# Performance work log

Measured on AMD Instinct MI355X. Metric: run time of the kernel, lower is better.

The kernel has to match this reference:

```python
import jax, jax.numpy as jnp
import numpy as np

D_MODEL, N_LEVELS, N_HEADS, N_POINTS = 256, 4, 8, 4
HEAD_DIM = D_MODEL // N_HEADS
SPATIAL = [(100, 100), (50, 50), (25, 25), (13, 13)]  # (H, W) per level
BATCH = 2


def setup_inputs() -> dict:
    key = jax.random.key(0)
    ks = jax.random.split(key, 10)
    len_in = sum(h * w for h, w in SPATIAL)
    n, lq = BATCH, len_in
    s = 0.02
    mlp = N_HEADS * N_LEVELS * N_POINTS
    starts = np.cumsum([0] + [h * w for h, w in SPATIAL])[:-1]
    return {
        "query": jax.random.normal(ks[0], (n, lq, D_MODEL), jnp.float32),
        "reference_points": jax.random.uniform(ks[1], (n, lq, N_LEVELS, 2), jnp.float32),
        "input_flatten": jax.random.normal(ks[2], (n, len_in, D_MODEL), jnp.float32),
        "input_spatial_shapes": jnp.array(SPATIAL, dtype=jnp.int32),
        "input_level_start_index": jnp.array(starts, dtype=jnp.int32),
        "Wv": jax.random.normal(ks[3], (D_MODEL, D_MODEL), jnp.float32) * s,
        "bv": jnp.zeros((D_MODEL,), jnp.float32),
        "Woff": jax.random.normal(ks[4], (D_MODEL, mlp * 2), jnp.float32) * s,
        "boff": jax.random.normal(ks[5], (mlp * 2,), jnp.float32) * s,
        "Wattn": jax.random.normal(ks[6], (D_MODEL, mlp), jnp.float32) * s,
        "battn": jnp.zeros((mlp,), jnp.float32),
        "Wout": jax.random.normal(ks[7], (D_MODEL, D_MODEL), jnp.float32) * s,
        "bout": jnp.zeros((D_MODEL,), jnp.float32),
    }


def _ms_deform_attn_core(value, spatial_shapes, loc, aw):
    """value [N,S,M,D]; loc [N,Lq,M,L,P,2] in [0,1]; aw [N,Lq,M,L,P] -> [N,Lq,M*D].
    Faithful to F.grid_sample(mode='bilinear', padding_mode='zeros', align_corners=False)."""
    n, lq, m, L, p, _ = loc.shape
    d = value.shape[-1]
    out = jnp.zeros((n, m, lq, d), value.dtype)
    gather = jax.vmap(jax.vmap(lambda v, i: v[i]))  # vmap over N and M
    start = 0
    for lvl, (H, W) in enumerate(spatial_shapes):
        v = value[:, start:start + H * W].transpose(0, 2, 1, 3)  # [N,M,HW,D]
        start += H * W
        # align_corners=False: grid g=2*loc-1 -> pixel = ((g+1)*size-1)/2 = loc*size-0.5
        x = loc[:, :, :, lvl, :, 0] * W - 0.5  # [N,Lq,M,P]
        y = loc[:, :, :, lvl, :, 1] * H - 0.5
        x0 = jnp.floor(x)
        y0 = jnp.floor(y)
        wx = x - x0
        wy = y - y0
        x0i = x0.astype(jnp.int32)
        y0i = y0.astype(jnp.int32)
        samp = jnp.zeros((n, m, lq * p, d), value.dtype)
        for dy, wyc in ((0, 1.0 - wy), (1, wy)):
            for dx, wxc in ((0, 1.0 - wx), (1, wx)):
                xi = x0i + dx
                yi = y0i + dy
                valid = (xi >= 0) & (xi < W) & (yi >= 0) & (yi < H)  # zeros padding
                idx = jnp.clip(yi, 0, H - 1) * W + jnp.clip(xi, 0, W - 1)
                idx = idx.transpose(0, 2, 1, 3).reshape(n, m, lq * p)
                w = (wxc * wyc * valid).transpose(0, 2, 1, 3).reshape(n, m, lq * p)
                samp = samp + gather(v, idx) * w[..., None]
        samp = samp.reshape(n, m, lq, p, d)
        aw_l = aw[:, :, :, lvl, :].transpose(0, 2, 1, 3)  # [N,M,Lq,P]
        out = out + (samp * aw_l[..., None]).sum(3)
    return out.transpose(0, 2, 1, 3).reshape(n, lq, m * d)


def reference(query, reference_points, input_flatten, input_spatial_shapes,
              input_level_start_index, Wv, bv, Woff, boff, Wattn, battn, Wout, bout):
    n, lq, _ = query.shape
    m, L, p = N_HEADS, N_LEVELS, N_POINTS
    shapes = np.asarray(input_spatial_shapes)  # concrete/static [L,2] = (H,W)
    value = (input_flatten @ Wv + bv).reshape(n, -1, m, HEAD_DIM)
    off = (query @ Woff + boff).reshape(n, lq, m, L, p, 2)
    aw = jax.nn.softmax((query @ Wattn + battn).reshape(n, lq, m, L * p), axis=-1)
    aw = aw.reshape(n, lq, m, L, p)
    norm = jnp.asarray(shapes[:, ::-1].astype(np.float32))  # [L,2] = (W,H)
    loc = reference_points[:, :, None, :, None, :] + off / norm[None, None, None, :, None, :]
    out = _ms_deform_attn_core(value, [tuple(s) for s in shapes.tolist()], loc, aw)
    return out @ Wout + bout
```

## Files before the change

kernel.cpp:

```cpp
#include <hip/hip_runtime.h>
#include <hip/hip_bf16.h>

#define NB    2
#define LQ    13294
#define DM    256
#define NH    8
#define HD    32
#define NL    4
#define NP    4
#define ROWS  (NB*LQ)

#define OFF_VALUE 0u
#define OFF_TMP   13613056u
#define OFF_OFFS  27226112u
#define OFF_AWL   54452224u
#define OFF_WT    61258752u
#define OFF_FLAG  61717504u

#define WT_WV    0
#define WT_WOFF  65536
#define WT_WATTN 131072
#define WT_WOUT  163840

typedef __attribute__((ext_vector_type(8))) short short8;
typedef __attribute__((ext_vector_type(4))) float floatx4;

static __device__ __forceinline__ float blo(int u)  { return __uint_as_float(((unsigned)u) << 16); }
static __device__ __forceinline__ float bhif(int u) { return __uint_as_float(((unsigned)u) & 0xffff0000u); }

static __device__ __forceinline__ int pack_bf2(float a, float b) {
    __hip_bfloat162 h(__float2bfloat16(a), __float2bfloat16(b));
    int u; __builtin_memcpy(&u, &h, 4); return u;
}

static __device__ __forceinline__ void gload_lds16(const void* g, void* l) {
    __builtin_amdgcn_global_load_lds(
        (const __attribute__((address_space(1))) unsigned*)g,
        (__attribute__((address_space(3))) unsigned*)l, 16, 0, 0);
}

__global__ void sniff_k(const unsigned int* __restrict__ q, int* __restrict__ flag) {
    const int t = threadIdx.x;
    int hits = 0;
#pragma unroll
    for (int i = 0; i < 4; ++i) {
        unsigned lo = q[t * 4 + i] & 0xffffu;
        unsigned e  = (lo >> 7) & 0xffu;
        if ((e >= 110u && e <= 132u) || lo == 0u) ++hits;
    }
#pragma unroll
    for (int s = 1; s < 64; s <<= 1) hits += __shfl_xor(hits, s);
    if (t == 0) *flag = (hits > 160) ? 1 : 0;
}

__global__ __launch_bounds__(256) void trans_k(
    const void* __restrict__ s0, const void* __restrict__ s1,
    const void* __restrict__ s2, const void* __restrict__ s3,
    short* __restrict__ wt, const int* __restrict__ flagp)
{
    const int flag = *flagp;
    const int z = blockIdx.z;
    const void* src = (z == 0) ? s0 : (z == 1) ? s1 : (z == 2) ? s2 : s3;
    short* dst = wt + ((z == 0) ? WT_WV : (z == 1) ? WT_WOFF : (z == 2) ? WT_WATTN : WT_WOUT);
    const int N = (z == 2) ? 128 : 256;
    const int n0 = blockIdx.x * 32, k0 = blockIdx.y * 32;
    if (n0 >= N) return;

    __shared__ short tile[32 * 36];
    const int t = threadIdx.x;
    const int r = t >> 3, c4 = (t & 7) * 4;
    if (flag) {
        const short* sp = (const short*)src + (k0 + r) * N + n0 + c4;
        *(short4*)&tile[r * 36 + c4] = *(const short4*)sp;
    } else {
        const float* sp = (const float*)src + (k0 + r) * N + n0 + c4;
        float4 v = *(const float4*)sp;
        short4 o;
        o.x = (short)(pack_bf2(v.x, v.x) & 0xffff);
        o.y = (short)(pack_bf2(v.y, v.y) & 0xffff);
        o.z = (short)(pack_bf2(v.z, v.z) & 0xffff);
        o.w = (short)(pack_bf2(v.w, v.w) & 0xffff);
        *(short4*)&tile[r * 36 + c4] = o;
    }
    __syncthreads();
    const int nn = t >> 3, r4 = (t & 7) * 4;
    short4 o;
    o.x = tile[(r4 + 0) * 36 + nn];
    o.y = tile[(r4 + 1) * 36 + nn];
    o.z = tile[(r4 + 2) * 36 + nn];
    o.w = tile[(r4 + 3) * 36 + nn];
    *(short4*)&dst[(n0 + nn) * 256 + k0 + r4] = o;
}

static __device__ __forceinline__ void gemm_body(
    const void* __restrict__ A, const short* __restrict__ Wt,
    const void* __restrict__ bias, const void* __restrict__ bias2,
    void* __restrict__ C, void* __restrict__ C2,
    const int M, const int Nn, const bool a_bf, const int c_mode,
    const int flag, const int bx, const int by,
    short* __restrict__ As, short* __restrict__ Bs)
{
    const int tid = threadIdx.x;
    const int w = tid >> 6, lane = tid & 63;
    const int qd = lane >> 4, ln = lane & 15;
    const int bm = by * 128, bn = bx * 128;
    const int wm = (w & 1) * 64, wn = (w >> 1) * 64;

    const int ar0 = tid >> 2,         ak0 = (tid & 3) * 8;
    const int ar1 = (tid + 256) >> 2, ak1 = (tid & 3) * 8;
    const int ga0 = min(bm + ar0, M - 1), ga1 = min(bm + ar1, M - 1);
    short* lA0 = As + w * 512;
    short* lA1 = As + 2048 + w * 512;
    short* lB0 = Bs + w * 512;
    short* lB1 = Bs + 2048 + w * 512;

    floatx4 acc[4][4];
#pragma unroll
    for (int i = 0; i < 4; ++i)
#pragma unroll
        for (int j = 0; j < 4; ++j) acc[i][j] = floatx4{0.f, 0.f, 0.f, 0.f};

    const short* Ab = (const short*)A;
    const float* Af = (const float*)A;

    for (int k0 = 0; k0 < 256; k0 += 32) {
        __syncthreads();
        gload_lds16(Wt + (bn + ar0) * 256 + k0 + ak0, lB0);
        gload_lds16(Wt + (bn + ar1) * 256 + k0 + ak1, lB1);
        if (a_bf) {
            gload_lds16(Ab + ga0 * 256 + k0 + ak0, lA0);
            gload_lds16(Ab + ga1 * 256 + k0 + ak1, lA1);
        } else {
            float4 f0 = *(const float4*)(Af + ga0 * 256 + k0 + ak0);
            float4 f1 = *(const float4*)(Af + ga0 * 256 + k0 + ak0 + 4);
            int4 p0; p0.x = pack_bf2(f0.x, f0.y); p0.y = pack_bf2(f0.z, f0.w);
                     p0.z = pack_bf2(f1.x, f1.y); p0.w = pack_bf2(f1.z, f1.w);
            *(int4*)&As[ar0 * 32 + ak0] = p0;
            float4 g0 = *(const float4*)(Af + ga1 * 256 + k0 + ak1);
            float4 g1 = *(const float4*)(Af + ga1 * 256 + k0 + ak1 + 4);
            int4 p1; p1.x = pack_bf2(g0.x, g0.y); p1.y = pack_bf2(g0.z, g0.w);
                     p1.z = pack_bf2(g1.x, g1.y); p1.w = pack_bf2(g1.z, g1.w);
            *(int4*)&As[ar1 * 32 + ak1] = p1;
        }
        __syncthreads();

        short8 af[4], bf[4];
#pragma unroll
        for (int i = 0; i < 4; ++i)
            af[i] = *(const short8*)&As[(wm + i * 16 + ln) * 32 + qd * 8];
#pragma unroll
        for (int j = 0; j < 4; ++j)
            bf[j] = *(const short8*)&Bs[(wn + j * 16 + ln) * 32 + qd * 8];
#pragma unroll
        for (int i = 0; i < 4; ++i)
#pragma unroll
            for (int j = 0; j < 4; ++j)
                acc[i][j] = __builtin_amdgcn_mfma_f32_16x16x32_bf16(af[i], bf[j], acc[i][j], 0, 0, 0);
    }

#pragma unroll
    for (int j = 0; j < 4; ++j) {
        const int col = bn + wn + j * 16 + ln;
        float bj;
        if (c_mode == 3 && col >= 256) {
            if (flag) bj = __bfloat162float(((const __hip_bfloat16*)bias2)[col - 256]);
            else      bj = ((const float*)bias2)[col - 256];
        } else {
            if (flag) bj = __bfloat162float(((const __hip_bfloat16*)bias)[col]);
            else      bj = ((const float*)bias)[col];
        }
#pragma unroll
        for (int i = 0; i < 4; ++i) {
#pragma unroll
            for (int r = 0; r < 4; ++r) {
                const int row = bm + wm + i * 16 + qd * 4 + r;
                if (row >= M) continue;
                const float v = acc[i][j][r] + bj;
                if (c_mode == 0)      ((__hip_bfloat16*)C)[row * Nn + col] = __float2bfloat16(v);
                else if (c_mode == 1) ((float*)C)[row * Nn + col] = v;
                else if (c_mode == 2) {
                    if (flag) ((__hip_bfloat16*)C)[row * Nn + col] = __float2bfloat16(v);
                    else      ((float*)C)[row * Nn + col] = v;
                } else {
                    if (col < 256) ((float*)C)[row * 256 + col] = v;
                    else           ((__hip_bfloat16*)C2)[row * 128 + col - 256] = __float2bfloat16(v);
                }
            }
        }
    }
}

__global__ __launch_bounds__(256) void gemm_lds_k(
    const void* __restrict__ A, const short* __restrict__ Wt,
    const void* __restrict__ bias, const void* __restrict__ bias2,
    void* __restrict__ C, void* __restrict__ C2,
    int M, int Nn, int a_mode, int c_mode, const int* __restrict__ flagp)
{
    __shared__ __align__(16) short As[128 * 32];
    __shared__ __align__(16) short Bs[128 * 32];
    const int flag = *flagp;
    const bool a_bf = (a_mode == 2) ? (flag != 0) : true;
    gemm_body(A, Wt, bias, bias2, C, C2, M, Nn, a_bf, c_mode, flag,
              blockIdx.x, blockIdx.y, As, Bs);
}

__global__ __launch_bounds__(256) void gemm_fused_k(
    const void* __restrict__ flat, const void* __restrict__ query,
    const short* __restrict__ wt,
    const void* __restrict__ bv, const void* __restrict__ boff,
    const void* __restrict__ battn,
    void* __restrict__ value, void* __restrict__ offsb, void* __restrict__ awl,
    const int* __restrict__ flagp)
{
    __shared__ __align__(16) short As[128 * 32];
    __shared__ __align__(16) short Bs[128 * 32];
    const int flag = *flagp;
    const bool a_bf = (flag != 0);
    if (blockIdx.z == 0) {
        if (blockIdx.x >= 2) return;
        gemm_body(flat, wt + WT_WV, bv, nullptr, value, nullptr,
                  ROWS, 256, a_bf, 0, flag, blockIdx.x, blockIdx.y, As, Bs);
    } else {
        gemm_body(query, wt + WT_WOFF, boff, battn, offsb, awl,
                  ROWS, 384, a_bf, 3, flag, blockIdx.x, blockIdx.y, As, Bs);
    }
}

__global__ __launch_bounds__(256) void sampler_k(
    const void* __restrict__ refp, const short* __restrict__ value,
    const float* __restrict__ offs, const short* __restrict__ awl,
    short* __restrict__ tmp, const int* __restrict__ flagp)
{
    const int flag = *flagp;
    const int wq = threadIdx.x >> 6;
    const int nq = blockIdx.x * 4 + wq;
    const int lane = threadIdx.x & 63;
    const int h = lane >> 3, u = lane & 7;
    const int n = (nq >= LQ) ? 1 : 0;

    __shared__ int2 recs[4][16][9][5];

    const int lg = *(const int*)(awl + nq * 128 + h * 16 + u * 2);
    float l0 = blo(lg), l1 = bhif(lg);
    float m = fmaxf(l0, l1);
    m = fmaxf(m, __shfl_xor(m, 1));
    m = fmaxf(m, __shfl_xor(m, 2));
    m = fmaxf(m, __shfl_xor(m, 4));
    float e0 = __expf(l0 - m), e1 = __expf(l1 - m);
    float s = e0 + e1;
    s += __shfl_xor(s, 1);
    s += __shfl_xor(s, 2);
    s += __shfl_xor(s, 4);
    const float inv = 1.f / s;
    const float w0 = e0 * inv, w1 = e1 * inv;

    const float4 of = *(const float4*)(offs + nq * 256 + h * 32 + u * 4);

    float rxl, ryl;
    if (flag) {
        const int rr = *(const int*)((const short*)refp + nq * 8 + (u & 3) * 2);
        rxl = blo(rr); ryl = bhif(rr);
    } else {
        const float* rp = (const float*)refp + nq * 8 + (u & 3) * 2;
        rxl = rp[0]; ryl = rp[1];
    }

    const int l = u >> 1;
    const int Wl = (0x0D193264 >> (l * 8)) & 0xff;
    const int St = (l == 0) ? 0 : (l == 1) ? 10000 : (l == 2) ? 12500 : 13125;
    const int rowbase = n * LQ + St;
    const float Wf = (float)Wl;
    const float rx = __shfl(rxl, h * 8 + l);
    const float ry = __shfl(ryl, h * 8 + l);

#pragma unroll
    for (int j = 0; j < 2; ++j) {
        const float ox = j ? of.z : of.x;
        const float oy = j ? of.w : of.y;
        const float wa = j ? w1 : w0;
        const float px = fmaf(rx, Wf, ox) - 0.5f;
        const float py = fmaf(ry, Wf, oy) - 0.5f;
        const float x0f = floorf(px), y0f = floorf(py);
        const float wx = px - x0f, wy = py - y0f;
        const int x0 = (int)x0f, y0 = (int)y0f;
        const float wxc[2] = {1.f - wx, wx};
        const float wyc[2] = {1.f - wy, wy};
#pragma unroll
        for (int dy = 0; dy < 2; ++dy) {
#pragma unroll
            for (int dx = 0; dx < 2; ++dx) {
                const int xi = x0 + dx, yi = y0 + dy;
                const bool vld = ((unsigned)xi < (unsigned)Wl) & ((unsigned)yi < (unsigned)Wl);
                int row = rowbase + yi * Wl + xi;
                row = vld ? row : rowbase;
                const float ww = vld ? wa * wxc[dx] * wyc[dy] : 0.f;
                recs[wq][u * 2 + j][h][dy * 2 + dx] =
                    make_int2(row << 9, __float_as_int(ww));
            }
        }
    }

    __syncthreads();

    const int laneoff = h * 64 + u * 8;
    const char* vb = (const char*)value;
    float a0 = 0.f, a1 = 0.f, a2 = 0.f, a3 = 0.f;

    int2  rA[8], rB[8];
    float wA[8], wB[8];

#define CHUNK(RW, WW, kk)                                                 \
    _Pragma("unroll")                                                     \
    for (int j = 0; j < 8; ++j) {                                         \
        const int2 rr = recs[wq][(kk) * 2 + (j >> 2)][h][j & 3];          \
        WW[j] = __int_as_float(rr.y);                                     \
        RW[j] = *(const int2*)(vb + (unsigned)(rr.x + laneoff));          \
    }
#define EAT(RW, WW)                                                       \
    _Pragma("unroll")                                                     \
    for (int j = 0; j < 8; ++j) {                                         \
        a0 = fmaf(WW[j], blo(RW[j].x),  a0);                              \
        a1 = fmaf(WW[j], bhif(RW[j].x), a1);                              \
        a2 = fmaf(WW[j], blo(RW[j].y),  a2);                              \
        a3 = fmaf(WW[j], bhif(RW[j].y), a3);                              \
    }

    CHUNK(rA, wA, 0)
    CHUNK(rB, wB, 1)
    EAT(rA, wA)  CHUNK(rA, wA, 2)
    EAT(rB, wB)  CHUNK(rB, wB, 3)
    EAT(rA, wA)  CHUNK(rA, wA, 4)
    EAT(rB, wB)  CHUNK(rB, wB, 5)
    EAT(rA, wA)  CHUNK(rA, wA, 6)
    EAT(rB, wB)  CHUNK(rB, wB, 7)
    EAT(rA, wA)
    EAT(rB, wB)
#undef CHUNK
#undef EAT

    int2 o;
    o.x = pack_bf2(a0, a1);
    o.y = pack_bf2(a2, a3);
    *(int2*)(tmp + nq * 256 + h * 32 + u * 4) = o;
}

extern "C" void kernel_launch(void* const* d_in, const int* in_sizes, int n_in,
                              void* d_out, int out_size, void* d_ws, size_t ws_size,
                              hipStream_t stream)
{
    const void* query  = d_in[0];
    const void* refpts = d_in[1];
    const void* flat   = d_in[2];
    const void* Wv     = d_in[5];
    const void* bv     = d_in[6];
    const void* Woff   = d_in[7];
    const void* boff   = d_in[8];
    const void* Wattn  = d_in[9];
    const void* battn  = d_in[10];
    const void* Wout   = d_in[11];
    const void* bout   = d_in[12];

    char* ws = (char*)d_ws;
    short* value = (short*)(ws + OFF_VALUE);
    short* tmp   = (short*)(ws + OFF_TMP);
    float* offsb = (float*)(ws + OFF_OFFS);
    short* awl   = (short*)(ws + OFF_AWL);
    short* wt    = (short*)(ws + OFF_WT);
    int*   flagp = (int*)(ws + OFF_FLAG);

    const int gmy = (ROWS + 127) / 128;

    sniff_k<<<1, 64, 0, stream>>>((const unsigned int*)query, flagp);
    trans_k<<<dim3(8, 8, 4), 256, 0, stream>>>(Wv, Woff, Wattn, Wout, wt, flagp);
    gemm_fused_k<<<dim3(3, gmy, 2), 256, 0, stream>>>(flat, query, wt, bv, boff, battn,
                                                      value, offsb, awl, flagp);
    sampler_k<<<ROWS / 4, 256, 0, stream>>>(refpts, value, offsb, awl, tmp, flagp);
    gemm_lds_k<<<dim3(2, gmy), 256, 0, stream>>>(tmp, wt + WT_WOUT, bout, nullptr,
                                                 d_out, nullptr, ROWS, 256, 1, 2, flagp);
}
```

Baseline: 229.3 us.

## Fuse all stages into one persistent cooperative kernel with grid syncs

Replaces the five separate launches (sniff, weight transpose, fused input GEMMs, sampler, output GEMM) with one cooperative persistent kernel that loops over work items and separates the stages with grid-wide syncs. Stage bodies are factored into device functions that share one LDS buffer. The aim is to remove per-launch overhead and inter-kernel gaps. In exchange, occupancy is capped at the occupancy-derived block count, grid syncs add their own cost, and the grid-stride loops may balance work worse than the original launches did; the multi-kernel path stays as a fallback.

New measurement: 231.5 us. Within noise of the previous version (+0.9%).

```diff
diff --git a/kernel.cpp b/kernel.cpp
--- a/kernel.cpp
+++ b/kernel.cpp
@@ -1,5 +1,8 @@
 #include <hip/hip_runtime.h>
 #include <hip/hip_bf16.h>
+#include <hip/hip_cooperative_groups.h>
+
+namespace cg = cooperative_groups;
 
 #define NB    2
 #define LQ    13294
@@ -39,8 +42,8 @@
         (__attribute__((address_space(3))) unsigned*)l, 16, 0, 0);
 }
 
-__global__ void sniff_k(const unsigned int* __restrict__ q, int* __restrict__ flag) {
-    const int t = threadIdx.x;
+static __device__ __forceinline__ void sniff_core(const unsigned* __restrict__ q,
+                                                  int* __restrict__ flag, int t) {
     int hits = 0;
 #pragma unroll
     for (int i = 0; i < 4; ++i) {
@@ -53,20 +56,21 @@
     if (t == 0) *flag = (hits > 160) ? 1 : 0;
 }
 
-__global__ __launch_bounds__(256) void trans_k(
+__global__ void sniff_k(const unsigned int* __restrict__ q, int* __restrict__ flag) {
+    sniff_core(q, flag, threadIdx.x);
+}
+
+static __device__ __forceinline__ void trans_core(
+    int z, int bx, int by, int flag,
     const void* __restrict__ s0, const void* __restrict__ s1,
     const void* __restrict__ s2, const void* __restrict__ s3,
-    short* __restrict__ wt, const int* __restrict__ flagp)
-{
-    const int flag = *flagp;
-    const int z = blockIdx.z;
+    short* __restrict__ wt, short* __restrict__ tile )
+{
     const void* src = (z == 0) ? s0 : (z == 1) ? s1 : (z == 2) ? s2 : s3;
     short* dst = wt + ((z == 0) ? WT_WV : (z == 1) ? WT_WOFF : (z == 2) ? WT_WATTN : WT_WOUT);
     const int N = (z == 2) ? 128 : 256;
-    const int n0 = blockIdx.x * 32, k0 = blockIdx.y * 32;
-    if (n0 >= N) return;
-
-    __shared__ short tile[32 * 36];
+    const int n0 = bx * 32, k0 = by * 32;
+
     const int t = threadIdx.x;
     const int r = t >> 3, c4 = (t & 7) * 4;
     if (flag) {
@@ -90,6 +94,18 @@
     o.z = tile[(r4 + 2) * 36 + nn];
     o.w = tile[(r4 + 3) * 36 + nn];
     *(short4*)&dst[(n0 + nn) * 256 + k0 + r4] = o;
+}
+
+__global__ __launch_bounds__(256) void trans_k(
+    const void* __restrict__ s0, const void* __restrict__ s1,
+    const void* __restrict__ s2, const void* __restrict__ s3,
+    short* __restrict__ wt, const int* __restrict__ flagp)
+{
+    __shared__ short tile[32 * 36];
+    const int z = blockIdx.z;
+    const int N = (z == 2) ? 128 : 256;
+    if ((int)blockIdx.x * 32 >= N) return;
+    trans_core(z, blockIdx.x, blockIdx.y, *flagp, s0, s1, s2, s3, wt, tile);
 }
 
 static __device__ __forceinline__ void gemm_body(
@@ -226,19 +242,14 @@
     }
 }
 
-__global__ __launch_bounds__(256) void sampler_k(
+static __device__ __forceinline__ void sampler_core(
+    const int nq, const int lane, const int flag,
     const void* __restrict__ refp, const short* __restrict__ value,
     const float* __restrict__ offs, const short* __restrict__ awl,
-    short* __restrict__ tmp, const int* __restrict__ flagp)
-{
-    const int flag = *flagp;
-    const int wq = threadIdx.x >> 6;
-    const int nq = blockIdx.x * 4 + wq;
-    const int lane = threadIdx.x & 63;
+    short* __restrict__ tmp, int2* __restrict__ recs)
+{
     const int h = lane >> 3, u = lane & 7;
     const int n = (nq >= LQ) ? 1 : 0;
-
-    __shared__ int2 recs[4][16][9][5];
 
     const int lg = *(const int*)(awl + nq * 128 + h * 16 + u * 2);
     float l0 = blo(lg), l1 = bhif(lg);
@@ -294,7 +305,7 @@
                 int row = rowbase + yi * Wl + xi;
                 row = vld ? row : rowbase;
                 const float ww = vld ? wa * wxc[dx] * wyc[dy] : 0.f;
-                recs[wq][u * 2 + j][h][dy * 2 + dx] =
+                recs[((u * 2 + j) * 9 + h) * 5 + dy * 2 + dx] =
                     make_int2(row << 9, __float_as_int(ww));
             }
         }
@@ -312,7 +323,7 @@
 #define CHUNK(RW, WW, kk)                                                 \
     _Pragma("unroll")                                                     \
     for (int j = 0; j < 8; ++j) {                                         \
-        const int2 rr = recs[wq][(kk) * 2 + (j >> 2)][h][j & 3];          \
+        const int2 rr = recs[(((kk) * 2 + (j >> 2)) * 9 + h) * 5 + (j & 3)]; \
         WW[j] = __int_as_float(rr.y);                                     \
         RW[j] = *(const int2*)(vb + (unsigned)(rr.x + laneoff));          \
     }
@@ -344,6 +355,81 @@
     *(int2*)(tmp + nq * 256 + h * 32 + u * 4) = o;
 }
 
+__global__ __launch_bounds__(256) void sampler_k(
+    const void* __restrict__ refp, const short* __restrict__ value,
+    const float* __restrict__ offs, const short* __restrict__ awl,
+    short* __restrict__ tmp, const int* __restrict__ flagp)
+{
+    __shared__ int2 recs[4][16][9][5];
+    const int wq = threadIdx.x >> 6;
+    sampler_core(blockIdx.x * 4 + wq, threadIdx.x & 63, *flagp,
+                 refp, value, offs, awl, tmp, &recs[wq][0][0][0]);
+}
+
+__global__ __launch_bounds__(256) void mega_k(
+    const void* __restrict__ query, const void* __restrict__ refpts,
+    const void* __restrict__ flat,
+    const void* __restrict__ Wv,   const void* __restrict__ bv,
+    const void* __restrict__ Woff, const void* __restrict__ boff,
+    const void* __restrict__ Wattn,const void* __restrict__ battn,
+    const void* __restrict__ Wout, const void* __restrict__ bout,
+    void* __restrict__ dout, char* __restrict__ ws)
+{
+    __shared__ __align__(16) char smem[23040];
+
+    short* value = (short*)(ws + OFF_VALUE);
+    short* tmp   = (short*)(ws + OFF_TMP);
+    float* offsb = (float*)(ws + OFF_OFFS);
+    short* awl   = (short*)(ws + OFF_AWL);
+    short* wt    = (short*)(ws + OFF_WT);
+    int*   flagp = (int*)(ws + OFF_FLAG);
+
+    const int bid = blockIdx.x, G = gridDim.x, tid = threadIdx.x;
+    cg::grid_group gg = cg::this_grid();
+
+    if (bid == 0 && tid < 64) sniff_core((const unsigned*)query, flagp, tid);
+    gg.sync();
+    const int flag = *flagp;
+
+    for (int j = bid; j < 224; j += G) {
+        int z, x, y;
+        if (j < 64)       { z = 0; x = j & 7;         y = j >> 3; }
+        else if (j < 128) { z = 1; x = (j - 64) & 7;  y = (j - 64) >> 3; }
+        else if (j < 160) { z = 2; x = (j - 128) & 3; y = (j - 128) >> 2; }
+        else              { z = 3; x = (j - 160) & 7; y = (j - 160) >> 3; }
+        trans_core(z, x, y, flag, Wv, Woff, Wattn, Wout, wt, (short*)smem);
+        __syncthreads();
+    }
+    gg.sync();
+
+    short* As = (short*)smem;
+    short* Bs = (short*)(smem + 8192);
+    const bool a_bf = (flag != 0);
+    for (int j = bid; j < 1040; j += G) {
+        if (j < 416) {
+            gemm_body(flat, wt + WT_WV, bv, nullptr, value, nullptr,
+                      ROWS, 256, a_bf, 0, flag, j & 1, j >> 1, As, Bs);
+        } else {
+            const int t2 = j - 416;
+            gemm_body(query, wt + WT_WOFF, boff, battn, offsb, awl,
+                      ROWS, 384, a_bf, 3, flag, t2 % 3, t2 / 3, As, Bs);
+        }
+    }
+    gg.sync();
+
+    {
+        int2* recbase = (int2*)smem + (tid >> 6) * (16 * 9 * 5);
+        const int wq = tid >> 6, lane = tid & 63;
+        for (int j = bid; j < ROWS / 4; j += G)
+            sampler_core(j * 4 + wq, lane, flag, refpts, value, offsb, awl, tmp, recbase);
+    }
+    gg.sync();
+
+    for (int j = bid; j < 416; j += G)
+        gemm_body(tmp, wt + WT_WOUT, bout, nullptr, dout, nullptr,
+                  ROWS, 256, true, 2, flag, j & 1, j >> 1, As, Bs);
+}
+
 extern "C" void kernel_launch(void* const* d_in, const int* in_sizes, int n_in,
                               void* d_out, int out_size, void* d_ws, size_t ws_size,
                               hipStream_t stream)
@@ -368,8 +454,32 @@
     short* wt    = (short*)(ws + OFF_WT);
     int*   flagp = (int*)(ws + OFF_FLAG);
 
+    static int gblocks = 0;
+    if (gblocks == 0) {
+        int nb = 0;
+        hipError_t qe = hipOccupancyMaxActiveBlocksPerMultiprocessor(
+            &nb, reinterpret_cast<const void*>(&mega_k), 256, 0);
+        if (qe != hipSuccess || nb < 1) gblocks = -1;
+        else {
+            gblocks = nb * 256;
+            if (gblocks > 2048) gblocks = 2048;
+        }
+    }
+
+    if (gblocks > 0) {
+        void* args[] = {
+            (void*)&query, (void*)&refpts, (void*)&flat,
+            (void*)&Wv, (void*)&bv, (void*)&Woff, (void*)&boff,
+            (void*)&Wattn, (void*)&battn, (void*)&Wout, (void*)&bout,
+            (void*)&d_out, (void*)&ws };
+        hipError_t e = hipLaunchCooperativeKernel(
+            reinterpret_cast<const void*>(&mega_k),
+            dim3((unsigned)gblocks), dim3(256), args, 0, stream);
+        if (e == hipSuccess) return;
+        gblocks = -1;
+    }
+
     const int gmy = (ROWS + 127) / 128;
-
     sniff_k<<<1, 64, 0, stream>>>((const unsigned int*)query, flagp);
     trans_k<<<dim3(8, 8, 4), 256, 0, stream>>>(Wv, Woff, Wattn, Wout, wt, flagp);
     gemm_fused_k<<<dim3(3, gmy, 2), 256, 0, stream>>>(flat, query, wt, bv, boff, battn,
```

## Double-buffer GEMM LDS staging and pre-convert fp32 inputs to bf16

Applied to the files above, without the earlier changes.

The GEMM main loop now uses two LDS buffers and issues the loads for the next K-slice before computing on the current one, which cuts one barrier per iteration and overlaps memory with MFMA. When the workspace is large enough, a new conv_k kernel first converts the fp32 flat and query inputs to bf16. The input GEMMs can then use direct global-to-LDS loads instead of converting in registers. This adds an extra pass over both inputs and doubles LDS use per block, which may lower occupancy.

New measurement: 235.9 us. 1.03x slower.

```diff
diff --git a/kernel.cpp b/kernel.cpp
--- a/kernel.cpp
+++ b/kernel.cpp
@@ -16,6 +16,9 @@
 #define OFF_AWL   54452224u
 #define OFF_WT    61258752u
 #define OFF_FLAG  61717504u
+#define OFF_FBF   61717632u
+#define OFF_QBF   75330688u
+#define WS_NEED   88943744u
 
 #define WT_WV    0
 #define WT_WOFF  65536
@@ -51,6 +54,25 @@
 #pragma unroll
     for (int s = 1; s < 64; s <<= 1) hits += __shfl_xor(hits, s);
     if (t == 0) *flag = (hits > 160) ? 1 : 0;
+}
+
+__global__ __launch_bounds__(256) void conv_k(
+    const float* __restrict__ fa, const float* __restrict__ fb,
+    short* __restrict__ oa, short* __restrict__ ob,
+    const int* __restrict__ flagp)
+{
+    if (*flagp) return;
+    const int total = ROWS * 256 / 8;
+    for (int i = blockIdx.x * 256 + threadIdx.x; i < total; i += gridDim.x * 256) {
+        float4 a0 = ((const float4*)fa)[i * 2], a1 = ((const float4*)fa)[i * 2 + 1];
+        int4 p; p.x = pack_bf2(a0.x, a0.y); p.y = pack_bf2(a0.z, a0.w);
+                p.z = pack_bf2(a1.x, a1.y); p.w = pack_bf2(a1.z, a1.w);
+        ((int4*)oa)[i] = p;
+        float4 b0 = ((const float4*)fb)[i * 2], b1 = ((const float4*)fb)[i * 2 + 1];
+        int4 q; q.x = pack_bf2(b0.x, b0.y); q.y = pack_bf2(b0.z, b0.w);
+                q.z = pack_bf2(b1.x, b1.y); q.w = pack_bf2(b1.z, b1.w);
+        ((int4*)ob)[i] = q;
+    }
 }
 
 __global__ __launch_bounds__(256) void trans_k(
@@ -96,9 +118,10 @@
     const void* __restrict__ A, const short* __restrict__ Wt,
     const void* __restrict__ bias, const void* __restrict__ bias2,
     void* __restrict__ C, void* __restrict__ C2,
-    const int M, const int Nn, const bool a_bf, const int c_mode,
+    const int M, const int Nn, const bool stage_f32, const int c_mode,
     const int flag, const int bx, const int by,
-    short* __restrict__ As, short* __restrict__ Bs)
+    short* __restrict__ As0, short* __restrict__ As1,
+    short* __restrict__ Bs0, short* __restrict__ Bs1)
 {
     const int tid = threadIdx.x;
     const int w = tid >> 6, lane = tid & 63;
@@ -106,13 +129,9 @@
     const int bm = by * 128, bn = bx * 128;
     const int wm = (w & 1) * 64, wn = (w >> 1) * 64;
 
-    const int ar0 = tid >> 2,         ak0 = (tid & 3) * 8;
-    const int ar1 = (tid + 256) >> 2, ak1 = (tid & 3) * 8;
+    const int ar0 = tid >> 2, ar1 = ar0 + 64;
+    const int ak  = (tid & 3) * 8;
     const int ga0 = min(bm + ar0, M - 1), ga1 = min(bm + ar1, M - 1);
-    short* lA0 = As + w * 512;
-    short* lA1 = As + 2048 + w * 512;
-    short* lB0 = Bs + w * 512;
-    short* lB1 = Bs + 2048 + w * 512;
 
     floatx4 acc[4][4];
 #pragma unroll
@@ -123,39 +142,50 @@
     const short* Ab = (const short*)A;
     const float* Af = (const float*)A;
 
-    for (int k0 = 0; k0 < 256; k0 += 32) {
-        __syncthreads();
-        gload_lds16(Wt + (bn + ar0) * 256 + k0 + ak0, lB0);
-        gload_lds16(Wt + (bn + ar1) * 256 + k0 + ak1, lB1);
-        if (a_bf) {
-            gload_lds16(Ab + ga0 * 256 + k0 + ak0, lA0);
-            gload_lds16(Ab + ga1 * 256 + k0 + ak1, lA1);
+    auto stage = [&](int kk, short* Ad, short* Bd) {
+        const int k0 = kk * 32;
+        gload_lds16(Wt + (bn + ar0) * 256 + k0 + ak, Bd + w * 512);
+        gload_lds16(Wt + (bn + ar1) * 256 + k0 + ak, Bd + 2048 + w * 512);
+        if (!stage_f32) {
+            gload_lds16(Ab + ga0 * 256 + k0 + ak, Ad + w * 512);
+            gload_lds16(Ab + ga1 * 256 + k0 + ak, Ad + 2048 + w * 512);
         } else {
-            float4 f0 = *(const float4*)(Af + ga0 * 256 + k0 + ak0);
-            float4 f1 = *(const float4*)(Af + ga0 * 256 + k0 + ak0 + 4);
+            float4 f0 = *(const float4*)(Af + ga0 * 256 + k0 + ak);
+            float4 f1 = *(const float4*)(Af + ga0 * 256 + k0 + ak + 4);
             int4 p0; p0.x = pack_bf2(f0.x, f0.y); p0.y = pack_bf2(f0.z, f0.w);
                      p0.z = pack_bf2(f1.x, f1.y); p0.w = pack_bf2(f1.z, f1.w);
-            *(int4*)&As[ar0 * 32 + ak0] = p0;
-            float4 g0 = *(const float4*)(Af + ga1 * 256 + k0 + ak1);
-            float4 g1 = *(const float4*)(Af + ga1 * 256 + k0 + ak1 + 4);
+            *(int4*)&Ad[ar0 * 32 + ak] = p0;
+            float4 g0 = *(const float4*)(Af + ga1 * 256 + k0 + ak);
+            float4 g1 = *(const float4*)(Af + ga1 * 256 + k0 + ak + 4);
             int4 p1; p1.x = pack_bf2(g0.x, g0.y); p1.y = pack_bf2(g0.z, g0.w);
                      p1.z = pack_bf2(g1.x, g1.y); p1.w = pack_bf2(g1.z, g1.w);
-            *(int4*)&As[ar1 * 32 + ak1] = p1;
+            *(int4*)&Ad[ar1 * 32 + ak] = p1;
         }
-        __syncthreads();
-
-        short8 af[4], bf[4];
+    };
+
+    stage(0, As0, Bs0);
+    __syncthreads();
+
+#pragma unroll
+    for (int kk = 0; kk < 8; ++kk) {
+        short* Ac = (kk & 1) ? As1 : As0;
+        short* Bc = (kk & 1) ? Bs1 : Bs0;
+        if (kk < 7) stage(kk + 1, (kk & 1) ? As0 : As1, (kk & 1) ? Bs0 : Bs1);
+
+        short8 af[4], bfr[4];
 #pragma unroll
         for (int i = 0; i < 4; ++i)
-            af[i] = *(const short8*)&As[(wm + i * 16 + ln) * 32 + qd * 8];
+            af[i] = *(const short8*)&Ac[(wm + i * 16 + ln) * 32 + qd * 8];
 #pragma unroll
         for (int j = 0; j < 4; ++j)
-            bf[j] = *(const short8*)&Bs[(wn + j * 16 + ln) * 32 + qd * 8];
+            bfr[j] = *(const short8*)&Bc[(wn + j * 16 + ln) * 32 + qd * 8];
 #pragma unroll
         for (int i = 0; i < 4; ++i)
 #pragma unroll
             for (int j = 0; j < 4; ++j)
-                acc[i][j] = __builtin_amdgcn_mfma_f32_16x16x32_bf16(af[i], bf[j], acc[i][j], 0, 0, 0);
+                acc[i][j] = __builtin_amdgcn_mfma_f32_16x16x32_bf16(af[i], bfr[j], acc[i][j], 0, 0, 0);
+
+        if (kk < 7) __syncthreads();
     }
 
 #pragma unroll
@@ -194,35 +224,36 @@
     const void* __restrict__ A, const short* __restrict__ Wt,
     const void* __restrict__ bias, const void* __restrict__ bias2,
     void* __restrict__ C, void* __restrict__ C2,
-    int M, int Nn, int a_mode, int c_mode, const int* __restrict__ flagp)
-{
-    __shared__ __align__(16) short As[128 * 32];
-    __shared__ __align__(16) short Bs[128 * 32];
-    const int flag = *flagp;
-    const bool a_bf = (a_mode == 2) ? (flag != 0) : true;
-    gemm_body(A, Wt, bias, bias2, C, C2, M, Nn, a_bf, c_mode, flag,
-              blockIdx.x, blockIdx.y, As, Bs);
+    int M, int Nn, int c_mode, const int* __restrict__ flagp)
+{
+    __shared__ __align__(16) short As0[4096], As1[4096], Bs0[4096], Bs1[4096];
+    gemm_body(A, Wt, bias, bias2, C, C2, M, Nn, false, c_mode, *flagp,
+              blockIdx.x, blockIdx.y, As0, As1, Bs0, Bs1);
 }
 
 __global__ __launch_bounds__(256) void gemm_fused_k(
-    const void* __restrict__ flat, const void* __restrict__ query,
+    const void* __restrict__ flat, const void* __restrict__ flatbf,
+    const void* __restrict__ query, const void* __restrict__ querybf,
     const short* __restrict__ wt,
     const void* __restrict__ bv, const void* __restrict__ boff,
     const void* __restrict__ battn,
     void* __restrict__ value, void* __restrict__ offsb, void* __restrict__ awl,
-    const int* __restrict__ flagp)
-{
-    __shared__ __align__(16) short As[128 * 32];
-    __shared__ __align__(16) short Bs[128 * 32];
+    int big, const int* __restrict__ flagp)
+{
+    __shared__ __align__(16) short As0[4096], As1[4096], Bs0[4096], Bs1[4096];
     const int flag = *flagp;
-    const bool a_bf = (flag != 0);
+    const bool stage_f32 = (!flag) && (!big);
     if (blockIdx.z == 0) {
         if (blockIdx.x >= 2) return;
-        gemm_body(flat, wt + WT_WV, bv, nullptr, value, nullptr,
-                  ROWS, 256, a_bf, 0, flag, blockIdx.x, blockIdx.y, As, Bs);
+        const void* A = flag ? flat : (big ? flatbf : flat);
+        gemm_body(A, wt + WT_WV, bv, nullptr, value, nullptr,
+                  ROWS, 256, stage_f32, 0, flag, blockIdx.x, blockIdx.y,
+                  As0, As1, Bs0, Bs1);
     } else {
-        gemm_body(query, wt + WT_WOFF, boff, battn, offsb, awl,
-                  ROWS, 384, a_bf, 3, flag, blockIdx.x, blockIdx.y, As, Bs);
+        const void* A = flag ? query : (big ? querybf : query);
+        gemm_body(A, wt + WT_WOFF, boff, battn, offsb, awl,
+                  ROWS, 384, stage_f32, 3, flag, blockIdx.x, blockIdx.y,
+                  As0, As1, Bs0, Bs1);
     }
 }
 
@@ -293,9 +324,8 @@
                 const bool vld = ((unsigned)xi < (unsigned)Wl) & ((unsigned)yi < (unsigned)Wl);
                 int row = rowbase + yi * Wl + xi;
                 row = vld ? row : rowbase;
-                const float ww = vld ? wa * wxc[dx] * wyc[dy] : 0.f;
                 recs[wq][u * 2 + j][h][dy * 2 + dx] =
-                    make_int2(row << 9, __float_as_int(ww));
+                    make_int2(row << 9, __float_as_int(vld ? wa * wxc[dx] * wyc[dy] : 0.f));
             }
         }
     }
@@ -367,14 +397,21 @@
     short* awl   = (short*)(ws + OFF_AWL);
     short* wt    = (short*)(ws + OFF_WT);
     int*   flagp = (int*)(ws + OFF_FLAG);
-
+    short* fbf   = (short*)(ws + OFF_FBF);
+    short* qbf   = (short*)(ws + OFF_QBF);
+
+    const int big = (ws_size >= (size_t)WS_NEED) ? 1 : 0;
     const int gmy = (ROWS + 127) / 128;
 
     sniff_k<<<1, 64, 0, stream>>>((const unsigned int*)query, flagp);
+    if (big)
+        conv_k<<<1664, 256, 0, stream>>>((const float*)flat, (const float*)query,
+                                         fbf, qbf, flagp);
     trans_k<<<dim3(8, 8, 4), 256, 0, stream>>>(Wv, Woff, Wattn, Wout, wt, flagp);
-    gemm_fused_k<<<dim3(3, gmy, 2), 256, 0, stream>>>(flat, query, wt, bv, boff, battn,
-                                                      value, offsb, awl, flagp);
+    gemm_fused_k<<<dim3(3, gmy, 2), 256, 0, stream>>>(flat, fbf, query, qbf, wt,
+                                                      bv, boff, battn,
+                                                      value, offsb, awl, big, flagp);
     sampler_k<<<ROWS / 4, 256, 0, stream>>>(refpts, value, offsb, awl, tmp, flagp);
     gemm_lds_k<<<dim3(2, gmy), 256, 0, stream>>>(tmp, wt + WT_WOUT, bout, nullptr,
-                                                 d_out, nullptr, ROWS, 256, 1, 2, flagp);
-}
+                                                 d_out, nullptr, ROWS, 256, 2, flagp);
+}
```

## Replace LDS-tiled 128x128 GEMMs with single-wave 32x64 register-direct MFMA GEMM

Applied to the files above, without the earlier changes.

Replaces the shared-memory tiled 256-thread GEMM (128x128 tiles, global_load_lds staging, barriers) with a 64-thread kernel that loads A and B fragments directly from global memory into registers and computes 32x64 tiles. The fused value/offset projection launch is split into two separate launches, and the output projection uses the same kernel. The intent is to remove LDS staging and barrier overhead and to raise the block count for better occupancy. In exchange, global-memory traffic rises because there is no LDS reuse and the weight matrix is re-read per small tile.

Result: slower. 283.2 us (+23.5%).

```diff
diff --git a/kernel.cpp b/kernel.cpp
--- a/kernel.cpp
+++ b/kernel.cpp
@@ -31,12 +31,6 @@
 static __device__ __forceinline__ int pack_bf2(float a, float b) {
     __hip_bfloat162 h(__float2bfloat16(a), __float2bfloat16(b));
     int u; __builtin_memcpy(&u, &h, 4); return u;
-}
-
-static __device__ __forceinline__ void gload_lds16(const void* g, void* l) {
-    __builtin_amdgcn_global_load_lds(
-        (const __attribute__((address_space(1))) unsigned*)g,
-        (__attribute__((address_space(3))) unsigned*)l, 16, 0, 0);
 }
 
 __global__ void sniff_k(const unsigned int* __restrict__ q, int* __restrict__ flag) {
@@ -92,75 +86,73 @@
     *(short4*)&dst[(n0 + nn) * 256 + k0 + r4] = o;
 }
 
-static __device__ __forceinline__ void gemm_body(
+static __device__ __forceinline__ short8 ldA_f32(const float* p) {
+    float4 f0 = *(const float4*)p, f1 = *(const float4*)(p + 4);
+    int4 q; q.x = pack_bf2(f0.x, f0.y); q.y = pack_bf2(f0.z, f0.w);
+            q.z = pack_bf2(f1.x, f1.y); q.w = pack_bf2(f1.z, f1.w);
+    short8 r; __builtin_memcpy(&r, &q, 16); return r;
+}
+
+__global__ __launch_bounds__(64) void wgemm_k(
     const void* __restrict__ A, const short* __restrict__ Wt,
     const void* __restrict__ bias, const void* __restrict__ bias2,
     void* __restrict__ C, void* __restrict__ C2,
-    const int M, const int Nn, const bool a_bf, const int c_mode,
-    const int flag, const int bx, const int by,
-    short* __restrict__ As, short* __restrict__ Bs)
+    int M, int Nn, int a_mode, int c_mode, const int* __restrict__ flagp)
 {
-    const int tid = threadIdx.x;
-    const int w = tid >> 6, lane = tid & 63;
+    const int flag = *flagp;
+    const bool a_bf = (a_mode == 1) || (flag != 0);
+    const int lane = threadIdx.x;
     const int qd = lane >> 4, ln = lane & 15;
-    const int bm = by * 128, bn = bx * 128;
-    const int wm = (w & 1) * 64, wn = (w >> 1) * 64;
-
-    const int ar0 = tid >> 2,         ak0 = (tid & 3) * 8;
-    const int ar1 = (tid + 256) >> 2, ak1 = (tid & 3) * 8;
-    const int ga0 = min(bm + ar0, M - 1), ga1 = min(bm + ar1, M - 1);
-    short* lA0 = As + w * 512;
-    short* lA1 = As + 2048 + w * 512;
-    short* lB0 = Bs + w * 512;
-    short* lB1 = Bs + 2048 + w * 512;
-
-    floatx4 acc[4][4];
-#pragma unroll
-    for (int i = 0; i < 4; ++i)
-#pragma unroll
-        for (int j = 0; j < 4; ++j) acc[i][j] = floatx4{0.f, 0.f, 0.f, 0.f};
-
+    const int bm = blockIdx.y * 32, bn = blockIdx.x * 64;
+
+    const int ar0 = min(bm + ln, M - 1);
+    const int ar1 = min(bm + 16 + ln, M - 1);
     const short* Ab = (const short*)A;
     const float* Af = (const float*)A;
 
-    for (int k0 = 0; k0 < 256; k0 += 32) {
-        __syncthreads();
-        gload_lds16(Wt + (bn + ar0) * 256 + k0 + ak0, lB0);
-        gload_lds16(Wt + (bn + ar1) * 256 + k0 + ak1, lB1);
-        if (a_bf) {
-            gload_lds16(Ab + ga0 * 256 + k0 + ak0, lA0);
-            gload_lds16(Ab + ga1 * 256 + k0 + ak1, lA1);
-        } else {
-            float4 f0 = *(const float4*)(Af + ga0 * 256 + k0 + ak0);
-            float4 f1 = *(const float4*)(Af + ga0 * 256 + k0 + ak0 + 4);
-            int4 p0; p0.x = pack_bf2(f0.x, f0.y); p0.y = pack_bf2(f0.z, f0.w);
-                     p0.z = pack_bf2(f1.x, f1.y); p0.w = pack_bf2(f1.z, f1.w);
-            *(int4*)&As[ar0 * 32 + ak0] = p0;
-            float4 g0 = *(const float4*)(Af + ga1 * 256 + k0 + ak1);
-            float4 g1 = *(const float4*)(Af + ga1 * 256 + k0 + ak1 + 4);
-            int4 p1; p1.x = pack_bf2(g0.x, g0.y); p1.y = pack_bf2(g0.z, g0.w);
-                     p1.z = pack_bf2(g1.x, g1.y); p1.w = pack_bf2(g1.z, g1.w);
-            *(int4*)&As[ar1 * 32 + ak1] = p1;
-        }
-        __syncthreads();
-
-        short8 af[4], bf[4];
-#pragma unroll
-        for (int i = 0; i < 4; ++i)
-            af[i] = *(const short8*)&As[(wm + i * 16 + ln) * 32 + qd * 8];
-#pragma unroll
-        for (int j = 0; j < 4; ++j)
-            bf[j] = *(const short8*)&Bs[(wn + j * 16 + ln) * 32 + qd * 8];
-#pragma unroll
-        for (int i = 0; i < 4; ++i)
+    floatx4 acc[2][4];
+#pragma unroll
+    for (int i = 0; i < 2; ++i)
+#pragma unroll
+        for (int j = 0; j < 4; ++j) acc[i][j] = floatx4{0.f, 0.f, 0.f, 0.f};
+
+    if (a_bf) {
+#pragma unroll 2
+        for (int kk = 0; kk < 8; ++kk) {
+            const int k0 = kk * 32 + qd * 8;
+            short8 af0 = *(const short8*)(Ab + ar0 * 256 + k0);
+            short8 af1 = *(const short8*)(Ab + ar1 * 256 + k0);
+            short8 bf[4];
 #pragma unroll
             for (int j = 0; j < 4; ++j)
-                acc[i][j] = __builtin_amdgcn_mfma_f32_16x16x32_bf16(af[i], bf[j], acc[i][j], 0, 0, 0);
+                bf[j] = *(const short8*)(Wt + (bn + j * 16 + ln) * 256 + k0);
+#pragma unroll
+            for (int j = 0; j < 4; ++j) {
+                acc[0][j] = __builtin_amdgcn_mfma_f32_16x16x32_bf16(af0, bf[j], acc[0][j], 0, 0, 0);
+                acc[1][j] = __builtin_amdgcn_mfma_f32_16x16x32_bf16(af1, bf[j], acc[1][j], 0, 0, 0);
+            }
+        }
+    } else {
+#pragma unroll 2
+        for (int kk = 0; kk < 8; ++kk) {
+            const int k0 = kk * 32 + qd * 8;
+            short8 af0 = ldA_f32(Af + ar0 * 256 + k0);
+            short8 af1 = ldA_f32(Af + ar1 * 256 + k0);
+            short8 bf[4];
+#pragma unroll
+            for (int j = 0; j < 4; ++j)
+                bf[j] = *(const short8*)(Wt + (bn + j * 16 + ln) * 256 + k0);
+#pragma unroll
+            for (int j = 0; j < 4; ++j) {
+                acc[0][j] = __builtin_amdgcn_mfma_f32_16x16x32_bf16(af0, bf[j], acc[0][j], 0, 0, 0);
+                acc[1][j] = __builtin_amdgcn_mfma_f32_16x16x32_bf16(af1, bf[j], acc[1][j], 0, 0, 0);
+            }
+        }
     }
 
 #pragma unroll
     for (int j = 0; j < 4; ++j) {
-        const int col = bn + wn + j * 16 + ln;
+        const int col = bn + j * 16 + ln;
         float bj;
         if (c_mode == 3 && col >= 256) {
             if (flag) bj = __bfloat162float(((const __hip_bfloat16*)bias2)[col - 256]);
@@ -170,10 +162,10 @@
             else      bj = ((const float*)bias)[col];
         }
 #pragma unroll
-        for (int i = 0; i < 4; ++i) {
+        for (int i = 0; i < 2; ++i) {
 #pragma unroll
             for (int r = 0; r < 4; ++r) {
-                const int row = bm + wm + i * 16 + qd * 4 + r;
+                const int row = bm + i * 16 + qd * 4 + r;
                 if (row >= M) continue;
                 const float v = acc[i][j][r] + bj;
                 if (c_mode == 0)      ((__hip_bfloat16*)C)[row * Nn + col] = __float2bfloat16(v);
@@ -187,42 +179,6 @@
                 }
             }
         }
-    }
-}
-
-__global__ __launch_bounds__(256) void gemm_lds_k(
-    const void* __restrict__ A, const short* __restrict__ Wt,
-    const void* __restrict__ bias, const void* __restrict__ bias2,
-    void* __restrict__ C, void* __restrict__ C2,
-    int M, int Nn, int a_mode, int c_mode, const int* __restrict__ flagp)
-{
-    __shared__ __align__(16) short As[128 * 32];
-    __shared__ __align__(16) short Bs[128 * 32];
-    const int flag = *flagp;
-    const bool a_bf = (a_mode == 2) ? (flag != 0) : true;
-    gemm_body(A, Wt, bias, bias2, C, C2, M, Nn, a_bf, c_mode, flag,
-              blockIdx.x, blockIdx.y, As, Bs);
-}
-
-__global__ __launch_bounds__(256) void gemm_fused_k(
-    const void* __restrict__ flat, const void* __restrict__ query,
-    const short* __restrict__ wt,
-    const void* __restrict__ bv, const void* __restrict__ boff,
-    const void* __restrict__ battn,
-    void* __restrict__ value, void* __restrict__ offsb, void* __restrict__ awl,
-    const int* __restrict__ flagp)
-{
-    __shared__ __align__(16) short As[128 * 32];
-    __shared__ __align__(16) short Bs[128 * 32];
-    const int flag = *flagp;
-    const bool a_bf = (flag != 0);
-    if (blockIdx.z == 0) {
-        if (blockIdx.x >= 2) return;
-        gemm_body(flat, wt + WT_WV, bv, nullptr, value, nullptr,
-                  ROWS, 256, a_bf, 0, flag, blockIdx.x, blockIdx.y, As, Bs);
-    } else {
-        gemm_body(query, wt + WT_WOFF, boff, battn, offsb, awl,
-                  ROWS, 384, a_bf, 3, flag, blockIdx.x, blockIdx.y, As, Bs);
     }
 }
 
@@ -293,9 +249,8 @@
                 const bool vld = ((unsigned)xi < (unsigned)Wl) & ((unsigned)yi < (unsigned)Wl);
                 int row = rowbase + yi * Wl + xi;
                 row = vld ? row : rowbase;
-                const float ww = vld ? wa * wxc[dx] * wyc[dy] : 0.f;
                 recs[wq][u * 2 + j][h][dy * 2 + dx] =
-                    make_int2(row << 9, __float_as_int(ww));
+                    make_int2(row << 9, __float_as_int(vld ? wa * wxc[dx] * wyc[dy] : 0.f));
             }
         }
     }
@@ -368,13 +323,15 @@
     short* wt    = (short*)(ws + OFF_WT);
     int*   flagp = (int*)(ws + OFF_FLAG);
 
-    const int gmy = (ROWS + 127) / 128;
+    const int mt = (ROWS + 31) / 32;
 
     sniff_k<<<1, 64, 0, stream>>>((const unsigned int*)query, flagp);
     trans_k<<<dim3(8, 8, 4), 256, 0, stream>>>(Wv, Woff, Wattn, Wout, wt, flagp);
-    gemm_fused_k<<<dim3(3, gmy, 2), 256, 0, stream>>>(flat, query, wt, bv, boff, battn,
-                                                      value, offsb, awl, flagp);
+    wgemm_k<<<dim3(4, mt), 64, 0, stream>>>(flat, wt + WT_WV, bv, nullptr,
+                                            value, nullptr, ROWS, 256, 2, 0, flagp);
+    wgemm_k<<<dim3(6, mt), 64, 0, stream>>>(query, wt + WT_WOFF, boff, battn,
+                                            offsb, awl, ROWS, 384, 2, 3, flagp);
     sampler_k<<<ROWS / 4, 256, 0, stream>>>(refpts, value, offsb, awl, tmp, flagp);
-    gemm_lds_k<<<dim3(2, gmy), 256, 0, stream>>>(tmp, wt + WT_WOUT, bout, nullptr,
-                                                 d_out, nullptr, ROWS, 256, 1, 2, flagp);
-}
+    wgemm_k<<<dim3(4, mt), 64, 0, stream>>>(tmp, wt + WT_WOUT, bout, nullptr,
+                                            d_out, nullptr, ROWS, 256, 1, 2, flagp);
+}
```
